# Performance work log

Hardware: AMD Instinct MI355X
Metric: run time of the kernel (lower is better)

## Reference

```python
import jax, jax.numpy as jnp
import numpy as np

CURV = 0.9            # geoopt PoincareBall(0.9)
SQRT_C = CURV ** 0.5
MIN_NORM = 1e-15
PROJ_EPS = 4e-3       # geoopt float32 boundary eps
ATANH_EPS = 1e-7
COS_EPS = 1e-8        # torch.cosine_similarity eps


def _norm(x):
    return jnp.sqrt(jnp.maximum(jnp.sum(x * x, axis=-1, keepdims=True), MIN_NORM * MIN_NORM))


def _project(x):
    # project onto ball of radius (1-eps)/sqrt(c)
    n = jnp.maximum(_norm(x), MIN_NORM)
    maxnorm = (1.0 - PROJ_EPS) / SQRT_C
    return jnp.where(n > maxnorm, x / n * maxnorm, x)


def expmap0(u):
    n = jnp.maximum(_norm(u), MIN_NORM)
    gamma = jnp.tanh(SQRT_C * n) * u / (SQRT_C * n)
    return _project(gamma)


def mobius_add(x, y):
    c = CURV
    x2 = jnp.sum(x * x, axis=-1, keepdims=True)
    y2 = jnp.sum(y * y, axis=-1, keepdims=True)
    xy = jnp.sum(x * y, axis=-1, keepdims=True)
    num = (1.0 + 2.0 * c * xy + c * y2) * x + (1.0 - c * x2) * y
    den = 1.0 + 2.0 * c * xy + c * c * x2 * y2
    return num / jnp.maximum(den, MIN_NORM)


def pdist(x, y):
    # dist(x,y) = 2/sqrt(c) * artanh(sqrt(c) * ||(-x) (+) y||)
    d = mobius_add(-x, y)
    n = _norm(d)[..., 0]
    z = jnp.clip(SQRT_C * n, -1.0 + ATANH_EPS, 1.0 - ATANH_EPS)
    return 2.0 / SQRT_C * jnp.arctanh(z)


def cos_sim(a, b):
    na = jnp.maximum(jnp.sqrt(jnp.sum(a * a, axis=-1)), COS_EPS)
    nb = jnp.maximum(jnp.sqrt(jnp.sum(b * b, axis=-1)), COS_EPS)
    return jnp.sum(a * b, axis=-1) / (na * nb)


def setup_inputs() -> dict:
    key = jax.random.key(0)
    ks = jax.random.split(key, 11)
    B, L, Ls, C, Lc, H, R = 4, 512, 128, 20, 128, 768, 512
    s = 0.02  # keep projected embeddings in a realistic range
    return {
        "text_out": jax.random.normal(ks[0], (B, L, H), jnp.float32),
        "summary_out": jax.random.normal(ks[1], (B, Ls, H), jnp.float32),
        "candidate_out": jax.random.normal(ks[2], (B, C, Lc, H), jnp.float32),
        "W_d": jax.random.normal(ks[3], (H, R), jnp.float32) * s,
        "W_s": jax.random.normal(ks[4], (H, R), jnp.float32) * s,
        "W_c": jax.random.normal(ks[5], (H, R), jnp.float32) * s,
        "W_p": jax.random.normal(ks[6], (R, R), jnp.float32) * s,
        "conv_w1": jax.random.normal(ks[7], (1, H, R), jnp.float32) * s,
        "conv_b1": jax.random.normal(ks[8], (R,), jnp.float32) * s,
        "conv_w2": jax.random.normal(ks[9], (2, H, R), jnp.float32) * s,
        "conv_b2": jax.random.normal(ks[10], (R,), jnp.float32) * s,
    }


def _forward(text_out, summary_out, candidate_out, W_d, W_s, W_c, W_p,
             conv_w1, conv_b1, conv_w2, conv_b2):
    # --- document ---
    doc_emb = expmap0(text_out[:, 0, :] @ W_d)                       # [B,R]

    # NGramers (max_gram=2, eval mode so dropout is identity)
    x = text_out[:, 1:-1, :]                                         # [B,L-2,H]
    y1 = jax.nn.relu(jnp.einsum('blh,hr->blr', x, conv_w1[0]) + conv_b1)
    y2 = jax.nn.relu(jnp.einsum('blh,hr->blr', x[:, :-1], conv_w2[0])
                     + jnp.einsum('blh,hr->blr', x[:, 1:], conv_w2[1]) + conv_b2)
    gram = jnp.concatenate([y1, y2], axis=1)                         # [B,2L-5,R]

    doc_word_emb = expmap0(jnp.einsum('blr,rk->blk', gram, W_p))     # [B,T,R]
    doc_inter = 1.0 / pdist(doc_word_emb, doc_emb[:, None, :])       # [B,T]

    # --- summary ---
    summary_emb = expmap0(jnp.max(summary_out, axis=1) @ W_s)        # [B,R]
    summary_score = -pdist(summary_emb, doc_emb) ** 2                # [B]
    sum_inter = 1.0 / pdist(doc_word_emb, summary_emb[:, None, :])   # [B,T]
    summary_score = summary_score + cos_sim(doc_inter, sum_inter)    # [B]

    # --- candidates ---
    cand_emb = expmap0(jnp.einsum('bch,hr->bcr', jnp.max(candidate_out, axis=2), W_c))  # [B,C,R]
    score = -pdist(cand_emb, doc_emb[:, None, :]) ** 2               # [B,C]
    cand_inter = 1.0 / pdist(doc_word_emb[:, None, :, :], cand_emb[:, :, None, :])      # [B,C,T]
    score = score + cos_sim(doc_inter[:, None, :], cand_inter)       # [B,C]
    return score, summary_score


def reference(text_out, summary_out, candidate_out, W_d, W_s, W_c, W_p,
              conv_w1, conv_b1, conv_w2, conv_b2):
    return _forward(text_out, summary_out, candidate_out, W_d, W_s, W_c, W_p,
                    conv_w1, conv_b1, conv_w2, conv_b2)
```

## Files before the change

kernel.cpp:

```cpp
#include <hip/hip_runtime.h>
#include <math.h>

#define SQRTC  0.94868329805051381f
#define MAXN   (0.996f/SQRTC)
#define OME_CLIP (1.0f - 0.996f*0.996f)
#define TWO_OVER_SQRTC 2.1081851067789197f

typedef unsigned short u16;
typedef __attribute__((ext_vector_type(8))) short bf8;
typedef __attribute__((ext_vector_type(4))) float f4;

__device__ __forceinline__ u16 f2bf(float f){
    union { float f; unsigned int i; } v; v.f = f;
    unsigned int x = v.i;
    unsigned int lsb = (x >> 16) & 1u;
    x += 0x7fffu + lsb;
    return (u16)(x >> 16);
}
__device__ __forceinline__ float bf2f(u16 u){
    union { unsigned int i; float f; } v; v.i = ((unsigned int)u) << 16; return v.f;
}

__device__ __forceinline__ float pdist_stable(float ome_x, float ome_y, float t){
    float u = 1.0f - ome_x, v = 1.0f - ome_y;
    float den = fmaxf(1.0f - 1.8f*t + u*v, 1e-15f);
    float q = ome_x*ome_y/den;
    q = fminf(fmaxf(q, 2.0e-7f), 1.0f);
    float z = sqrtf(fmaxf(1.0f - q, 0.0f));
    float at = 0.5f * logf((1.0f+z)*(1.0f+z)/q);
    return TWO_OVER_SQRTC * at;
}

__device__ __forceinline__ void expmap_scale_ome(float sum, float* fout, float* omeout){
    float nraw = sqrtf(fmaxf(sum, 1e-30f));
    float n = fmaxf(nraw, 1e-15f);
    float sn = SQRTC*n;
    float th = tanhf(sn);
    float factor = th/sn;
    float gn = factor*nraw;
    if (gn > MAXN){ *fout = factor*(MAXN/gn); *omeout = OME_CLIP; }
    else { *fout = factor; *omeout = fmaxf((1.0f-th)*(1.0f+th), 1e-12f); }
}

__global__ __launch_bounds__(256)
void k_stage1(const float* __restrict__ summ, const float* __restrict__ cand,
              const float* __restrict__ text,
              const float* __restrict__ w1, const float* __restrict__ w2,
              const float* __restrict__ wp,
              float* __restrict__ smax, float* __restrict__ cmax,
              u16* __restrict__ textb, u16* __restrict__ w1t,
              u16* __restrict__ w2t, u16* __restrict__ wpt)
{
    __shared__ float shm[1056];
    int bx = blockIdx.x;
    int t = threadIdx.x;
    if (bx < 1008){
        int row = bx / 12, ht = bx - row*12;
        int lane = t & 63, lg = t >> 6;
        int h = ht*64 + lane;
        const float* in = (row < 4) ? (summ + (long long)row*128*768)
                                    : (cand + (long long)(row-4)*128*768);
        const float* p = in + (long long)(lg*32)*768 + h;
        float m = -INFINITY;
        #pragma unroll 8
        for (int l = 0; l < 32; l++) m = fmaxf(m, p[l*768]);
        shm[t] = m; __syncthreads();
        if (t < 64){
            float mm = fmaxf(fmaxf(shm[t], shm[t+64]), fmaxf(shm[t+128], shm[t+192]));
            if (row < 4) smax[row*768 + h] = mm;
            else cmax[(row-4)*768 + h] = mm;
        }
        return;
    }
    int pb = bx - 1008;
    if (pb < 768){
        int base = pb*2048 + t*8;
        float4 a = *(const float4*)(text + base);
        float4 b = *(const float4*)(text + base + 4);
        *(ushort4*)(textb + base)     = make_ushort4(f2bf(a.x), f2bf(a.y), f2bf(a.z), f2bf(a.w));
        *(ushort4*)(textb + base + 4) = make_ushort4(f2bf(b.x), f2bf(b.y), f2bf(b.z), f2bf(b.w));
        return;
    }
    int j = pb - 768;
    const float* in; u16* outp; int K;
    if (j < 384){ in = w1; outp = w1t; K = 768; }
    else if (j < 1152){ j -= 384; in = w2; outp = w2t; K = 1536; }
    else { j -= 1152; in = wp; outp = wpt; K = 512; }
    const int N = 512, ntile = N/32;
    int k0 = (j/ntile)*32, n0 = (j - (j/ntile)*ntile)*32;
    int tx = t & 31, ty = t >> 5;
    #pragma unroll
    for (int i = 0; i < 4; i++)
        shm[(ty*4+i)*33 + tx] = in[(long long)(k0 + ty*4 + i)*N + n0 + tx];
    __syncthreads();
    #pragma unroll
    for (int i = 0; i < 4; i++)
        outp[(long long)(n0 + ty*4 + i)*K + k0 + tx] = f2bf(shm[tx*33 + ty*4+i]);
}

__global__ __launch_bounds__(256)
void k_stage2(const u16* __restrict__ textb,
              const u16* __restrict__ w1t, const u16* __restrict__ w2t,
              const float* __restrict__ cb1, const float* __restrict__ cb2,
              const float* __restrict__ text,
              const float* __restrict__ smax, const float* __restrict__ cmax,
              const float* __restrict__ W_d, const float* __restrict__ W_s,
              const float* __restrict__ W_c,
              u16* __restrict__ gram, float* __restrict__ emb_all)
{
    __shared__ char smem[8192];
    int bx = blockIdx.x;
    int t = threadIdx.x;
    if (bx < 512){
        u16 (*As)[32] = (u16(*)[32])smem;
        u16 (*Bs)[32] = (u16(*)[32])(smem + 4096);
        int xx = bx & 63, yy = bx >> 6;
        int job = xx & 1;
        int m0 = (xx >> 1) * 64;
        int n0 = yy * 64;
        int K   = job ? 1536 : 768;
        int M   = job ? 2036 : 2040;
        int rpb = job ? 509 : 510;
        int ob  = job ? 510 : 0;
        const u16* Bt = job ? w2t : w1t;
        const float* bias = job ? cb2 : cb1;
        int sr = t >> 2, sk = (t & 3) << 3;
        const u16* Arow = nullptr;
        { int gm = m0 + sr; if (gm < M){ int b = gm/rpb, l = gm - b*rpb;
            Arow = textb + (long long)b*393216 + (long long)(l+1)*768; } }
        const u16* Brow = Bt + (long long)(n0 + sr)*K;
        int lane = t & 63, wv = t >> 6;
        int fm = lane & 15, fq = lane >> 4;
        int arow = wv*16 + fm;
        f4 acc0 = {0,0,0,0}, acc1 = {0,0,0,0}, acc2 = {0,0,0,0}, acc3 = {0,0,0,0};
        for (int k0 = 0; k0 < K; k0 += 32){
            bf8 av = {};
            if (Arow) av = *(const bf8*)(Arow + k0 + sk);
            bf8 bv = *(const bf8*)(Brow + k0 + sk);
            *(bf8*)&As[sr][sk] = av;
            *(bf8*)&Bs[sr][sk] = bv;
            __syncthreads();
            bf8 af = *(const bf8*)&As[arow][fq*8];
            bf8 b0 = *(const bf8*)&Bs[ 0+fm][fq*8];
            bf8 b1 = *(const bf8*)&Bs[16+fm][fq*8];
            bf8 b2 = *(const bf8*)&Bs[32+fm][fq*8];
            bf8 b3 = *(const bf8*)&Bs[48+fm][fq*8];
            acc0 = __builtin_amdgcn_mfma_f32_16x16x32_bf16(af, b0, acc0, 0, 0, 0);
            acc1 = __builtin_amdgcn_mfma_f32_16x16x32_bf16(af, b1, acc1, 0, 0, 0);
            acc2 = __builtin_amdgcn_mfma_f32_16x16x32_bf16(af, b2, acc2, 0, 0, 0);
            acc3 = __builtin_amdgcn_mfma_f32_16x16x32_bf16(af, b3, acc3, 0, 0, 0);
            __syncthreads();
        }
        int col = n0 + fm;
        float bv0 = bias[col], bv1 = bias[col+16], bv2 = bias[col+32], bv3 = bias[col+48];
        #pragma unroll
        for (int i = 0; i < 4; i++){
            int row = m0 + wv*16 + fq*4 + i;
            if (row >= M) continue;
            int b = row/rpb, l = row - b*rpb;
            long long orow = (long long)b*1019 + ob + l;
            u16* gp = gram + orow*512;
            gp[col]      = f2bf(fmaxf(acc0[i] + bv0, 0.f));
            gp[col + 16] = f2bf(fmaxf(acc1[i] + bv1, 0.f));
            gp[col + 32] = f2bf(fmaxf(acc2[i] + bv2, 0.f));
            gp[col + 48] = f2bf(fmaxf(acc3[i] + bv3, 0.f));
        }
        return;
    }
    {
        int eb = bx - 512;
        int row = eb >> 3, nt = eb & 7;
        float* a   = (float*)smem;
        float* red = (float*)smem + 768;
        const float* A; const float* W;
        if (row < 4){ A = text + (long long)row*512*768; W = W_d; }
        else if (row < 8){ A = smax + (long long)(row-4)*768; W = W_s; }
        else { A = cmax + (long long)(row-8)*768; W = W_c; }
        for (int k = t; k < 768; k += 256) a[k] = A[k];
        __syncthreads();
        int lane = t & 63, kg = t >> 6;
        int col = nt*64 + lane;
        const float* Wp = W + (long long)(kg*192)*512 + col;
        float acc = 0.f;
        #pragma unroll 8
        for (int k = 0; k < 192; k++) acc += a[kg*192 + k] * Wp[k*512];
        red[t] = acc; __syncthreads();
        if (t < 64) emb_all[(long long)row*512 + col] = red[t] + red[t+64] + red[t+128] + red[t+192];
    }
}

__global__ __launch_bounds__(256)
void k_stage3(const u16* __restrict__ gram, const u16* __restrict__ wpt,
              u16* __restrict__ dwe_b,
              float* __restrict__ emb_all, float* __restrict__ ome_all)
{
    __shared__ char smem[8192];
    int bx = blockIdx.x;
    int t = threadIdx.x;
    if (bx < 512){
        u16 (*As)[32] = (u16(*)[32])smem;
        u16 (*Bs)[32] = (u16(*)[32])(smem + 4096);
        const int K = 512, M = 4076;
        int m0 = (bx >> 3) * 64;
        int n0 = (bx & 7) * 64;
        int sr = t >> 2, sk = (t & 3) << 3;
        const u16* Arow = (m0 + sr < M) ? (gram + (long long)(m0 + sr)*512) : nullptr;
        const u16* Brow = wpt + (long long)(n0 + sr)*K;
        int lane = t & 63, wv = t >> 6;
        int fm = lane & 15, fq = lane >> 4;
        int arow = wv*16 + fm;
        f4 acc0 = {0,0,0,0}, acc1 = {0,0,0,0}, acc2 = {0,0,0,0}, acc3 = {0,0,0,0};
        for (int k0 = 0; k0 < K; k0 += 32){
            bf8 av = {};
            if (Arow) av = *(const bf8*)(Arow + k0 + sk);
            bf8 bv = *(const bf8*)(Brow + k0 + sk);
            *(bf8*)&As[sr][sk] = av;
            *(bf8*)&Bs[sr][sk] = bv;
            __syncthreads();
            bf8 af = *(const bf8*)&As[arow][fq*8];
            bf8 b0 = *(const bf8*)&Bs[ 0+fm][fq*8];
            bf8 b1 = *(const bf8*)&Bs[16+fm][fq*8];
            bf8 b2 = *(const bf8*)&Bs[32+fm][fq*8];
            bf8 b3 = *(const bf8*)&Bs[48+fm][fq*8];
            acc0 = __builtin_amdgcn_mfma_f32_16x16x32_bf16(af, b0, acc0, 0, 0, 0);
            acc1 = __builtin_amdgcn_mfma_f32_16x16x32_bf16(af, b1, acc1, 0, 0, 0);
            acc2 = __builtin_amdgcn_mfma_f32_16x16x32_bf16(af, b2, acc2, 0, 0, 0);
            acc3 = __builtin_amdgcn_mfma_f32_16x16x32_bf16(af, b3, acc3, 0, 0, 0);
            __syncthreads();
        }
        int col = n0 + fm;
        #pragma unroll
        for (int i = 0; i < 4; i++){
            int row = m0 + wv*16 + fq*4 + i;
            if (row >= M) continue;
            u16* dp = dwe_b + (long long)row*512;
            dp[col]      = f2bf(acc0[i]);
            dp[col + 16] = f2bf(acc1[i]);
            dp[col + 32] = f2bf(acc2[i]);
            dp[col + 48] = f2bf(acc3[i]);
        }
        return;
    }
    {
        float* red = (float*)smem;
        int row = bx - 512;
        float* X = emb_all + (long long)row*512;
        float2 u = *(float2*)(X + t*2);
        red[t] = u.x*u.x + u.y*u.y; __syncthreads();
        for (int s = 128; s > 0; s >>= 1){ if (t < s) red[t] += red[t+s]; __syncthreads(); }
        float f, ome;
        expmap_scale_ome(red[0], &f, &ome);
        *(float2*)(X + t*2) = make_float2(u.x*f, u.y*f);
        if (t == 0) ome_all[row] = ome;
    }
}

__global__ __launch_bounds__(64)
void k_dots(const u16* __restrict__ dwe_b,
            const float* __restrict__ emb_all, const float* __restrict__ ome_all,
            float* __restrict__ doc_inter, float* __restrict__ sum_inter,
            float* __restrict__ cand_inter)
{
    int row = blockIdx.x;
    int b = row / 1019;
    int l = row - b*1019;
    int lane = threadIdx.x;
    bf8 xr = *(const bf8*)(dwe_b + (long long)row*512 + lane*8);
    float x[8];
    #pragma unroll
    for (int j = 0; j < 8; j++) x[j] = bf2f(((u16*)&xr)[j]);
    float ss = 0.f;
    #pragma unroll
    for (int j = 0; j < 8; j++) ss += x[j]*x[j];
    #pragma unroll
    for (int off = 32; off > 0; off >>= 1) ss += __shfl_xor(ss, off, 64);
    float f, ox;
    expmap_scale_ome(ss, &f, &ox);
    #pragma unroll
    for (int j = 0; j < 8; j++) x[j] *= f;

    for (int c = 0; c < 22; c++){
        int ei = (c == 0) ? b : (c == 1) ? (4 + b) : (8 + b*20 + (c-2));
        const float* y = emb_all + (long long)ei*512 + lane*8;
        float oy = ome_all[ei];
        float4 y0 = *(const float4*)(y);
        float4 y1 = *(const float4*)(y + 4);
        float s = x[0]*y0.x + x[1]*y0.y + x[2]*y0.z + x[3]*y0.w
                + x[4]*y1.x + x[5]*y1.y + x[6]*y1.z + x[7]*y1.w;
        #pragma unroll
        for (int off = 32; off > 0; off >>= 1) s += __shfl_xor(s, off, 64);
        float dist = pdist_stable(ox, oy, s);
        if (lane == 0){
            float inv = 1.0f/fmaxf(dist, 1e-12f);
            if (c == 0) doc_inter[row] = inv;
            else if (c == 1) sum_inter[row] = inv;
            else cand_inter[((long long)(b*20 + (c-2)))*1019 + l] = inv;
        }
    }
}

__global__ __launch_bounds__(256)
void k_final(const float* __restrict__ doc_inter, const float* __restrict__ sum_inter,
             const float* __restrict__ cand_inter,
             const float* __restrict__ emb_all, const float* __restrict__ ome_all,
             float* __restrict__ out)
{
    __shared__ float r0[256], r1[256], r2[256], r3[256];
    int j = blockIdx.x, t = threadIdx.x;
    int b; const float *a, *bb; int xi, yi; int outIdx;
    if (j < 80){
        b = j/20;
        a  = doc_inter + b*1019;
        bb = cand_inter + (long long)j*1019;
        xi = 8 + j; yi = b;
        outIdx = j;
    } else {
        b = j - 80;
        a  = doc_inter + b*1019;
        bb = sum_inter + b*1019;
        xi = 4 + b; yi = b;
        outIdx = 80 + b;
    }
    const float* xe = emb_all + (long long)xi*512;
    const float* ye = emb_all + (long long)yi*512;
    float ox = ome_all[xi], oy = ome_all[yi];
    float saa = 0.f, sbb = 0.f, sab = 0.f, st = 0.f;
    for (int l = t; l < 1019; l += 256){ float av = a[l], bv = bb[l]; saa += av*av; sbb += bv*bv; sab += av*bv; }
    for (int k = t; k < 512; k += 256) st += xe[k]*ye[k];
    r0[t] = saa; r1[t] = sbb; r2[t] = sab; r3[t] = st; __syncthreads();
    for (int s = 128; s > 0; s >>= 1){
        if (t < s){ r0[t] += r0[t+s]; r1[t] += r1[t+s]; r2[t] += r2[t+s]; r3[t] += r3[t+s]; }
        __syncthreads();
    }
    if (t == 0){
        float na = fmaxf(sqrtf(r0[0]), 1e-8f);
        float nb = fmaxf(sqrtf(r1[0]), 1e-8f);
        float cosv = r2[0] / (na*nb);
        float pd = pdist_stable(ox, oy, r3[0]);
        out[outIdx] = -pd*pd + cosv;
    }
}

extern "C" void kernel_launch(void* const* d_in, const int* in_sizes, int n_in,
                              void* d_out, int out_size, void* d_ws, size_t ws_size,
                              hipStream_t stream) {
    const float* text = (const float*)d_in[0];
    const float* summ = (const float*)d_in[1];
    const float* cand = (const float*)d_in[2];
    const float* W_d  = (const float*)d_in[3];
    const float* W_s  = (const float*)d_in[4];
    const float* W_c  = (const float*)d_in[5];
    const float* W_p  = (const float*)d_in[6];
    const float* cw1  = (const float*)d_in[7];
    const float* cb1  = (const float*)d_in[8];
    const float* cw2  = (const float*)d_in[9];
    const float* cb2  = (const float*)d_in[10];
    float* out = (float*)d_out;

    const int B = 4, C = 20, H = 768;

    char* base = (char*)d_ws;
    size_t off = 0;
    auto allocF = [&](size_t n)->float*{ float* p = (float*)(base + off); off += ((n*4) + 255) & ~(size_t)255; return p; };
    auto allocU = [&](size_t n)->u16*{ u16* p = (u16*)(base + off); off += ((n*2) + 255) & ~(size_t)255; return p; };

    float* smax = allocF(B*H);
    float* cmax = allocF(B*C*H);
    float* emb_all = allocF(88*512);
    float* ome_all = allocF(88);
    u16* textb = allocU(4*512*768);
    u16* w1t   = allocU(512*768);
    u16* w2t   = allocU(512*1536);
    u16* wpt   = allocU(512*512);
    u16* gram  = allocU(4076*512);
    u16* dwe_b = allocU(4076*512);
    float* doc_inter = allocF(4076);
    float* sum_inter = allocF(4076);
    float* cand_inter= allocF(B*C*1019);

    k_stage1<<<3184, 256, 0, stream>>>(summ, cand, text, cw1, cw2, W_p,
                                       smax, cmax, textb, w1t, w2t, wpt);

    k_stage2<<<1216, 256, 0, stream>>>(textb, w1t, w2t, cb1, cb2,
                                       text, smax, cmax, W_d, W_s, W_c,
                                       gram, emb_all);

    k_stage3<<<600, 256, 0, stream>>>(gram, wpt, dwe_b, emb_all, ome_all);

    k_dots<<<4076, 64, 0, stream>>>(dwe_b, emb_all, ome_all,
                                    doc_inter, sum_inter, cand_inter);

    k_final<<<84, 256, 0, stream>>>(doc_inter, sum_inter, cand_inter,
                                    emb_all, ome_all, out);
}
```

Baseline: 168.6 us.

## Compute word-to-embedding dot products with bf16 MFMA tiles instead of per-row wave reductions

```diff
diff --git a/kernel.cpp b/kernel.cpp
--- a/kernel.cpp
+++ b/kernel.cpp
@@ -192,7 +192,8 @@
 __global__ __launch_bounds__(256)
 void k_stage3(const u16* __restrict__ gram, const u16* __restrict__ wpt,
               u16* __restrict__ dwe_b,
-              float* __restrict__ emb_all, float* __restrict__ ome_all)
+              float* __restrict__ emb_all, float* __restrict__ ome_all,
+              u16* __restrict__ emb_b)
 {
     __shared__ char smem[8192];
     int bx = blockIdx.x;
@@ -250,51 +251,85 @@
         for (int s = 128; s > 0; s >>= 1){ if (t < s) red[t] += red[t+s]; __syncthreads(); }
         float f, ome;
         expmap_scale_ome(red[0], &f, &ome);
-        *(float2*)(X + t*2) = make_float2(u.x*f, u.y*f);
+        float sx = u.x*f, sy = u.y*f;
+        *(float2*)(X + t*2) = make_float2(sx, sy);
+        u16* Xb = emb_b + (long long)row*512;
+        Xb[t*2]   = f2bf(sx);
+        Xb[t*2+1] = f2bf(sy);
         if (t == 0) ome_all[row] = ome;
     }
 }
 
-__global__ __launch_bounds__(64)
-void k_dots(const u16* __restrict__ dwe_b,
-            const float* __restrict__ emb_all, const float* __restrict__ ome_all,
-            float* __restrict__ doc_inter, float* __restrict__ sum_inter,
-            float* __restrict__ cand_inter)
+__global__ __launch_bounds__(256)
+void k_dots_mfma(const u16* __restrict__ dwe_b, const u16* __restrict__ emb_b,
+                 const float* __restrict__ ome_all,
+                 float* __restrict__ doc_inter, float* __restrict__ sum_inter,
+                 float* __restrict__ cand_inter)
 {
-    int row = blockIdx.x;
-    int b = row / 1019;
-    int l = row - b*1019;
-    int lane = threadIdx.x;
-    bf8 xr = *(const bf8*)(dwe_b + (long long)row*512 + lane*8);
-    float x[8];
+    __shared__ u16 As[64][32];
+    __shared__ u16 Bs[32][32];
+    __shared__ float ssp[64][4];
+    __shared__ float ssl[64];
+    __shared__ float oyl[22];
+    int bx = blockIdx.x;
+    int b  = bx >> 4;
+    int m0 = (bx & 15) * 64;
+    int t = threadIdx.x;
+    int sra = t >> 2, ska = (t & 3) << 3;
+    const u16* Arow = (m0 + sra < 1019) ? (dwe_b + (long long)(b*1019 + m0 + sra)*512) : nullptr;
+    const u16* Brow = nullptr;
+    if (t < 128){
+        int n = t >> 2;
+        if (n < 22){
+            int ei = (n == 0) ? b : (n == 1) ? 4 + b : 8 + b*20 + (n - 2);
+            Brow = emb_b + (long long)ei*512;
+        }
+    }
+    if (t < 22) oyl[t] = ome_all[(t == 0) ? b : (t == 1) ? 4 + b : 8 + b*20 + (t - 2)];
+    int lane = t & 63, wv = t >> 6;
+    int fm = lane & 15, fq = lane >> 4;
+    f4 acc0 = {0,0,0,0}, acc1 = {0,0,0,0};
+    float ssq = 0.f;
+    for (int k0 = 0; k0 < 512; k0 += 32){
+        bf8 av = {};
+        if (Arow) av = *(const bf8*)(Arow + k0 + ska);
+        *(bf8*)&As[sra][ska] = av;
+        if (t < 128){
+            bf8 bv = {};
+            if (Brow) bv = *(const bf8*)(Brow + k0 + ((t & 3) << 3));
+            *(bf8*)&Bs[t >> 2][(t & 3) << 3] = bv;
+        }
+        #pragma unroll
+        for (int j = 0; j < 8; j++){ float x = bf2f(((u16*)&av)[j]); ssq += x*x; }
+        __syncthreads();
+        bf8 af = *(const bf8*)&As[wv*16 + fm][fq*8];
+        bf8 b0 = *(const bf8*)&Bs[fm][fq*8];
+        bf8 b1 = *(const bf8*)&Bs[16 + fm][fq*8];
+        acc0 = __builtin_amdgcn_mfma_f32_16x16x32_bf16(af, b0, acc0, 0, 0, 0);
+        acc1 = __builtin_amdgcn_mfma_f32_16x16x32_bf16(af, b1, acc1, 0, 0, 0);
+        __syncthreads();
+    }
+    ssp[sra][t & 3] = ssq; __syncthreads();
+    if (t < 64) ssl[t] = ssp[t][0] + ssp[t][1] + ssp[t][2] + ssp[t][3];
+    __syncthreads();
     #pragma unroll
-    for (int j = 0; j < 8; j++) x[j] = bf2f(((u16*)&xr)[j]);
-    float ss = 0.f;
-    #pragma unroll
-    for (int j = 0; j < 8; j++) ss += x[j]*x[j];
-    #pragma unroll
-    for (int off = 32; off > 0; off >>= 1) ss += __shfl_xor(ss, off, 64);
-    float f, ox;
-    expmap_scale_ome(ss, &f, &ox);
-    #pragma unroll
-    for (int j = 0; j < 8; j++) x[j] *= f;
-
-    for (int c = 0; c < 22; c++){
-        int ei = (c == 0) ? b : (c == 1) ? (4 + b) : (8 + b*20 + (c-2));
-        const float* y = emb_all + (long long)ei*512 + lane*8;
-        float oy = ome_all[ei];
-        float4 y0 = *(const float4*)(y);
-        float4 y1 = *(const float4*)(y + 4);
-        float s = x[0]*y0.x + x[1]*y0.y + x[2]*y0.z + x[3]*y0.w
-                + x[4]*y1.x + x[5]*y1.y + x[6]*y1.z + x[7]*y1.w;
+    for (int i = 0; i < 4; i++){
+        int rtile = wv*16 + fq*4 + i;
+        int row = m0 + rtile;
+        if (row >= 1019) continue;
+        float f, ox;
+        expmap_scale_ome(ssl[rtile], &f, &ox);
+        long long grow = (long long)b*1019 + row;
         #pragma unroll
-        for (int off = 32; off > 0; off >>= 1) s += __shfl_xor(s, off, 64);
-        float dist = pdist_stable(ox, oy, s);
-        if (lane == 0){
+        for (int g = 0; g < 2; g++){
+            int c = g*16 + fm;
+            if (c >= 22) continue;
+            float s = (g ? acc1[i] : acc0[i]) * f;
+            float dist = pdist_stable(ox, oyl[c], s);
             float inv = 1.0f/fmaxf(dist, 1e-12f);
-            if (c == 0) doc_inter[row] = inv;
-            else if (c == 1) sum_inter[row] = inv;
-            else cand_inter[((long long)(b*20 + (c-2)))*1019 + l] = inv;
+            if (c == 0) doc_inter[grow] = inv;
+            else if (c == 1) sum_inter[grow] = inv;
+            else cand_inter[((long long)(b*20 + (c - 2)))*1019 + row] = inv;
         }
     }
 }
@@ -368,6 +403,7 @@
     float* cmax = allocF(B*C*H);
     float* emb_all = allocF(88*512);
     float* ome_all = allocF(88);
+    u16* emb_b = allocU(88*512);
     u16* textb = allocU(4*512*768);
     u16* w1t   = allocU(512*768);
     u16* w2t   = allocU(512*1536);
@@ -385,10 +421,10 @@
                                        text, smax, cmax, W_d, W_s, W_c,
                                        gram, emb_all);
 
-    k_stage3<<<600, 256, 0, stream>>>(gram, wpt, dwe_b, emb_all, ome_all);
-
-    k_dots<<<4076, 64, 0, stream>>>(dwe_b, emb_all, ome_all,
-                                    doc_inter, sum_inter, cand_inter);
+    k_stage3<<<600, 256, 0, stream>>>(gram, wpt, dwe_b, emb_all, ome_all, emb_b);
+
+    k_dots_mfma<<<64, 256, 0, stream>>>(dwe_b, emb_b, ome_all,
+                                        doc_inter, sum_inter, cand_inter);
 
     k_final<<<84, 256, 0, stream>>>(doc_inter, sum_inter, cand_inter,
                                     emb_all, ome_all, out);
```

After: 161.1 us. 4.5% less time.
